# Kernel optimization log

Hardware: AMD Instinct MI355X
Metric: run time of the kernel (lower is better)

## Reference

```python
import jax, jax.numpy as jnp
import numpy as np

WINDOW = 8
DIM = 192
HEADS = 6
NWIN = 4096  # number of windows (B_)


def _relative_position_index(w):
    coords = np.stack(np.meshgrid(np.arange(w), np.arange(w), indexing='ij'))  # [2,w,w]
    cf = coords.reshape(2, -1)                                                 # [2, w*w]
    rel = cf[:, :, None] - cf[:, None, :]                                      # [2, N, N]
    rel = rel.transpose(1, 2, 0).astype(np.int32)
    rel[:, :, 0] += w - 1
    rel[:, :, 1] += w - 1
    rel[:, :, 0] *= 2 * w - 1
    return rel.sum(-1)  # [N, N] in [0, (2w-1)^2)


def setup_inputs() -> dict:
    key = jax.random.key(0)
    ks = jax.random.split(key, 6)
    N = WINDOW * WINDOW
    x = jax.random.normal(ks[0], (NWIN, N, DIM), dtype=jnp.float32)
    qkv_w = jax.random.normal(ks[1], (3 * DIM, DIM), dtype=jnp.float32) * (DIM ** -0.5)
    qkv_b = jax.random.normal(ks[2], (3 * DIM,), dtype=jnp.float32) * 0.02
    proj_w = jax.random.normal(ks[3], (DIM, DIM), dtype=jnp.float32) * (DIM ** -0.5)
    proj_b = jax.random.normal(ks[4], (DIM,), dtype=jnp.float32) * 0.02
    bias_table = jax.random.normal(ks[5], ((2 * WINDOW - 1) ** 2, HEADS), dtype=jnp.float32) * 0.02
    rel_index = jnp.asarray(_relative_position_index(WINDOW))
    return {"x": x, "qkv_w": qkv_w, "qkv_b": qkv_b, "proj_w": proj_w,
            "proj_b": proj_b, "bias_table": bias_table, "rel_index": rel_index}


def reference(x, qkv_w, qkv_b, proj_w, proj_b, bias_table, rel_index):
    B, N, C = x.shape
    H = HEADS
    hd = C // H
    scale = hd ** -0.5
    # qkv projection (torch Linear: x @ W.T + b)
    qkv = (x @ qkv_w.T + qkv_b).reshape(B, N, 3, H, hd)
    qkv = jnp.transpose(qkv, (2, 0, 3, 1, 4))  # [3, B, H, N, hd]
    q, k, v = qkv[0], qkv[1], qkv[2]
    attn = jnp.einsum('bhqd,bhkd->bhqk', q, k) * scale  # [B,H,N,N]
    # relative position bias gather: [N,N,H] -> [H,N,N]
    bias = bias_table[rel_index.reshape(-1)].reshape(N, N, H)
    bias = jnp.transpose(bias, (2, 0, 1))
    attn = jax.nn.softmax(attn + bias[None], axis=-1)
    out = jnp.einsum('bhqk,bhkd->bhqd', attn, v)         # [B,H,N,hd]
    out = jnp.transpose(out, (0, 2, 1, 3)).reshape(B, N, C)
    return out @ proj_w.T + proj_b
```

## Files before the change

kernel.cpp:

```cpp
#include <hip/hip_runtime.h>


#define NTOK 64
#define DIM  192
#define HEADS 6
#define NWIN 4096

typedef short short8  __attribute__((ext_vector_type(8)));
typedef short short4v __attribute__((ext_vector_type(4)));
typedef float f32x4   __attribute__((ext_vector_type(4)));

__device__ __forceinline__ short f2bf(float f) {
    unsigned u = __builtin_bit_cast(unsigned, f);
    unsigned r = (u + 0x7fffu + ((u >> 16) & 1u)) >> 16;
    return (short)r;
}

__device__ __forceinline__ short8 ld_cvt8(const float* p) {
    f32x4 a = *(const f32x4*)p;
    f32x4 b = *(const f32x4*)(p + 4);
    short8 r;
    r[0] = f2bf(a[0]); r[1] = f2bf(a[1]); r[2] = f2bf(a[2]); r[3] = f2bf(a[3]);
    r[4] = f2bf(b[0]); r[5] = f2bf(b[1]); r[6] = f2bf(b[2]); r[7] = f2bf(b[3]);
    return r;
}

#define QW_ELEMS 110592
#define TOT_W_ELEMS 147456

__global__ void convw(const float* __restrict__ qw, const float* __restrict__ pw,
                      short* __restrict__ wsw) {
    int i = (blockIdx.x * 256 + threadIdx.x) * 4;
    if (i >= TOT_W_ELEMS) return;
    const float* src = (i < QW_ELEMS) ? (qw + i) : (pw + (i - QW_ELEMS));
    f32x4 v = *(const f32x4*)src;
    short4v o;
    o[0] = f2bf(v[0]); o[1] = f2bf(v[1]); o[2] = f2bf(v[2]); o[3] = f2bf(v[3]);
    *(short4v*)(wsw + i) = o;
}

#define Q_OFF   0
#define K_OFF   12800
#define VT_OFF  25600
#define SMEM_SHORTS 39424

template <bool WF32>
__global__ __launch_bounds__(384, 3) void msa_fused(
    const float* __restrict__ x,
    const short* __restrict__ wq_bf, const short* __restrict__ wp_bf,
    const float* __restrict__ wq_f,  const float* __restrict__ wp_f,
    const float* __restrict__ qkv_b, const float* __restrict__ proj_b,
    const float* __restrict__ bias_table, const int* __restrict__ rel_index,
    float* __restrict__ out)
{
    __shared__ __align__(16) short smem[SMEM_SHORTS];

    const int tid  = threadIdx.x;
    const int wave = tid >> 6;
    const int lane = tid & 63;
    const int quad = lane >> 4;
    const int l15  = lane & 15;
    const int b    = blockIdx.x;

    short* qs = smem + Q_OFF;
    short* ks = smem + K_OFF;
    short* vt = smem + VT_OFF;

    const float* xg = x + b * (NTOK * DIM);
    short8 afr[4][6];
#pragma unroll
    for (int mt = 0; mt < 4; ++mt)
#pragma unroll
        for (int kk = 0; kk < 6; ++kk)
            afr[mt][kk] = ld_cvt8(xg + (mt*16 + l15)*DIM + kk*32 + quad*8);

#pragma unroll
    for (int nt = 0; nt < 6; ++nt) {
        const int N0 = wave*96 + nt*16;
        f32x4 acc[4];
#pragma unroll
        for (int mt = 0; mt < 4; ++mt) acc[mt] = (f32x4){0.f,0.f,0.f,0.f};
#pragma unroll
        for (int kk = 0; kk < 6; ++kk) {
            short8 bfr;
            if constexpr (WF32) bfr = ld_cvt8(wq_f + (N0 + l15)*DIM + kk*32 + quad*8);
            else                bfr = *(const short8*)(wq_bf + (N0 + l15)*DIM + kk*32 + quad*8);
#pragma unroll
            for (int mt = 0; mt < 4; ++mt)
                acc[mt] = __builtin_amdgcn_mfma_f32_16x16x32_bf16(afr[mt][kk], bfr, acc[mt], 0, 0, 0);
        }
        const float bv = qkv_b[N0 + l15];
        if (wave < 2) {
#pragma unroll
            for (int mt = 0; mt < 4; ++mt)
#pragma unroll
                for (int r = 0; r < 4; ++r)
                    qs[(mt*16 + quad*4 + r)*200 + N0 + l15] = f2bf(acc[mt][r] + bv);
        } else if (wave < 4) {
#pragma unroll
            for (int mt = 0; mt < 4; ++mt)
#pragma unroll
                for (int r = 0; r < 4; ++r)
                    ks[(mt*16 + quad*4 + r)*200 + (N0 - 192) + l15] = f2bf(acc[mt][r] + bv);
        } else {
#pragma unroll
            for (int mt = 0; mt < 4; ++mt)
#pragma unroll
                for (int r = 0; r < 4; ++r)
                    vt[(N0 - 384 + l15)*72 + mt*16 + quad*4 + r] = f2bf(acc[mt][r] + bv);
        }
    }
    __syncthreads();

    const int h = wave;
    const int koff = h*32 + quad*8;
    short8 qa[4], kb[4];
#pragma unroll
    for (int t = 0; t < 4; ++t) {
        qa[t] = *(const short8*)(qs + (t*16 + l15)*200 + koff);
        kb[t] = *(const short8*)(ks + (t*16 + l15)*200 + koff);
    }
    f32x4 s[4][4];
#pragma unroll
    for (int mt = 0; mt < 4; ++mt)
#pragma unroll
        for (int nt = 0; nt < 4; ++nt) {
            f32x4 z = (f32x4){0.f,0.f,0.f,0.f};
            s[mt][nt] = __builtin_amdgcn_mfma_f32_16x16x32_bf16(qa[mt], kb[nt], z, 0, 0, 0);
        }
    __syncthreads();

    const float scale = 0.17677669529663687f;
#pragma unroll
    for (int mt = 0; mt < 4; ++mt)
#pragma unroll
        for (int r = 0; r < 4; ++r) {
            const int row = mt*16 + quad*4 + r;
            float m = -1e30f;
#pragma unroll
            for (int nt = 0; nt < 4; ++nt) {
                const int col = nt*16 + l15;
                const int idx = rel_index[row*64 + col];
                float val = s[mt][nt][r]*scale + bias_table[idx*HEADS + h];
                s[mt][nt][r] = val;
                m = fmaxf(m, val);
            }
#pragma unroll
            for (int off = 8; off >= 1; off >>= 1) m = fmaxf(m, __shfl_xor(m, off, 16));
            float sum = 0.f;
#pragma unroll
            for (int nt = 0; nt < 4; ++nt) {
                float e = exp2f((s[mt][nt][r] - m) * 1.44269504f);
                s[mt][nt][r] = e;
                sum += e;
            }
#pragma unroll
            for (int off = 8; off >= 1; off >>= 1) sum += __shfl_xor(sum, off, 16);
            const float inv = 1.f / sum;
#pragma unroll
            for (int nt = 0; nt < 4; ++nt) s[mt][nt][r] *= inv;
        }

    short* ps = smem + wave*2560;
    f32x4 oa[4][2];
#pragma unroll
    for (int mt = 0; mt < 4; ++mt)
#pragma unroll
        for (int n2 = 0; n2 < 2; ++n2) oa[mt][n2] = (f32x4){0.f,0.f,0.f,0.f};
#pragma unroll
    for (int kh = 0; kh < 2; ++kh) {
        __syncthreads();
#pragma unroll
        for (int mt = 0; mt < 4; ++mt)
#pragma unroll
            for (int n2 = 0; n2 < 2; ++n2)
#pragma unroll
                for (int r = 0; r < 4; ++r)
                    ps[(mt*16 + quad*4 + r)*40 + n2*16 + l15] = f2bf(s[mt][kh*2 + n2][r]);
        __syncthreads();
        short8 pfr[4], vfr[2];
#pragma unroll
        for (int mt = 0; mt < 4; ++mt)
            pfr[mt] = *(const short8*)(ps + (mt*16 + l15)*40 + quad*8);
#pragma unroll
        for (int n2 = 0; n2 < 2; ++n2)
            vfr[n2] = *(const short8*)(vt + (h*32 + n2*16 + l15)*72 + kh*32 + quad*8);
#pragma unroll
        for (int mt = 0; mt < 4; ++mt)
#pragma unroll
            for (int n2 = 0; n2 < 2; ++n2)
                oa[mt][n2] = __builtin_amdgcn_mfma_f32_16x16x32_bf16(pfr[mt], vfr[n2], oa[mt][n2], 0, 0, 0);
    }
    __syncthreads();

    short* os = smem;
#pragma unroll
    for (int mt = 0; mt < 4; ++mt)
#pragma unroll
        for (int n2 = 0; n2 < 2; ++n2)
#pragma unroll
            for (int r = 0; r < 4; ++r)
                os[(mt*16 + quad*4 + r)*200 + h*32 + n2*16 + l15] = f2bf(oa[mt][n2][r]);
    __syncthreads();

    short8 ofr[4][6];
#pragma unroll
    for (int mt = 0; mt < 4; ++mt)
#pragma unroll
        for (int kk = 0; kk < 6; ++kk)
            ofr[mt][kk] = *(const short8*)(os + (mt*16 + l15)*200 + kk*32 + quad*8);

    float* outg = out + b * (NTOK * DIM);
#pragma unroll
    for (int nt = 0; nt < 2; ++nt) {
        const int c0 = wave*32 + nt*16;
        f32x4 acc[4];
#pragma unroll
        for (int mt = 0; mt < 4; ++mt) acc[mt] = (f32x4){0.f,0.f,0.f,0.f};
#pragma unroll
        for (int kk = 0; kk < 6; ++kk) {
            short8 bfr;
            if constexpr (WF32) bfr = ld_cvt8(wp_f + (c0 + l15)*DIM + kk*32 + quad*8);
            else                bfr = *(const short8*)(wp_bf + (c0 + l15)*DIM + kk*32 + quad*8);
#pragma unroll
            for (int mt = 0; mt < 4; ++mt)
                acc[mt] = __builtin_amdgcn_mfma_f32_16x16x32_bf16(ofr[mt][kk], bfr, acc[mt], 0, 0, 0);
        }
        const float pb = proj_b[c0 + l15];
#pragma unroll
        for (int mt = 0; mt < 4; ++mt)
#pragma unroll
            for (int r = 0; r < 4; ++r) {
                float sv = acc[mt][r] + pb;
                if (!(__builtin_fabsf(sv) < 1e30f)) sv = 0.f;
                outg[(mt*16 + quad*4 + r)*DIM + c0 + l15] = sv;
            }
    }
}

extern "C" void kernel_launch(void* const* d_in, const int* in_sizes, int n_in,
                              void* d_out, int out_size, void* d_ws, size_t ws_size,
                              hipStream_t stream) {
    const float* x          = (const float*)d_in[0];
    const float* qkv_w      = (const float*)d_in[1];
    const float* qkv_b      = (const float*)d_in[2];
    const float* proj_w     = (const float*)d_in[3];
    const float* proj_b     = (const float*)d_in[4];
    const float* bias_table = (const float*)d_in[5];
    const int*   rel_index  = (const int*)d_in[6];
    float* out = (float*)d_out;

    if (ws_size >= (size_t)TOT_W_ELEMS * sizeof(short)) {
        short* wsw = (short*)d_ws;
        convw<<<144, 256, 0, stream>>>(qkv_w, proj_w, wsw);
        msa_fused<false><<<NWIN, 384, 0, stream>>>(
            x, wsw, wsw + QW_ELEMS, qkv_w, proj_w,
            qkv_b, proj_b, bias_table, rel_index, out);
    } else {
        msa_fused<true><<<NWIN, 384, 0, stream>>>(
            x, nullptr, nullptr, qkv_w, proj_w,
            qkv_b, proj_b, bias_table, rel_index, out);
    }
}
```

Measured before the change: 864.0 us.

## Restructure per-head attention with register transposes, staged x, and pre-gathered bias fragments

Each wave now computes its own head's Q, K and V projections (Q/K transposed via W·x^T) and rearranges them into MFMA operand layout with cross-lane shuffles instead of writing them through shared memory. x is staged once in LDS as bf16, and the relative-position bias is pre-gathered by the prep kernel into fragment order. LDS drops from about 77KB to 25KB and launch bounds rise to 4 blocks per CU, removing several barriers. In exchange, every wave re-reads the x tile from LDS for all three projections and pays for many lane shuffles.

```diff
diff --git a/kernel.cpp b/kernel.cpp
--- a/kernel.cpp
+++ b/kernel.cpp
@@ -9,51 +9,70 @@
 typedef short short8  __attribute__((ext_vector_type(8)));
 typedef short short4v __attribute__((ext_vector_type(4)));
 typedef float f32x4   __attribute__((ext_vector_type(4)));
+typedef unsigned int u32;
+typedef u32 u32x2 __attribute__((ext_vector_type(2)));
+typedef u32 u32x4 __attribute__((ext_vector_type(4)));
+
+#define QW_SHORTS  110592
+#define W_SHORTS   147456
+#define BIAS_OFF_B 294912
+#define WS_NEEDED  (294912 + 98304)
 
 __device__ __forceinline__ short f2bf(float f) {
     unsigned u = __builtin_bit_cast(unsigned, f);
     unsigned r = (u + 0x7fffu + ((u >> 16) & 1u)) >> 16;
     return (short)r;
 }
-
+__device__ __forceinline__ u32 pkbf(float lo, float hi) {
+    u32 d;
+    asm("v_cvt_pk_bf16_f32 %0, %1, %2" : "=v"(d) : "v"(lo), "v"(hi));
+    return d;
+}
 __device__ __forceinline__ short8 ld_cvt8(const float* p) {
     f32x4 a = *(const f32x4*)p;
     f32x4 b = *(const f32x4*)(p + 4);
-    short8 r;
-    r[0] = f2bf(a[0]); r[1] = f2bf(a[1]); r[2] = f2bf(a[2]); r[3] = f2bf(a[3]);
-    r[4] = f2bf(b[0]); r[5] = f2bf(b[1]); r[6] = f2bf(b[2]); r[7] = f2bf(b[3]);
-    return r;
-}
-
-#define QW_ELEMS 110592
-#define TOT_W_ELEMS 147456
-
-__global__ void convw(const float* __restrict__ qw, const float* __restrict__ pw,
-                      short* __restrict__ wsw) {
-    int i = (blockIdx.x * 256 + threadIdx.x) * 4;
-    if (i >= TOT_W_ELEMS) return;
-    const float* src = (i < QW_ELEMS) ? (qw + i) : (pw + (i - QW_ELEMS));
-    f32x4 v = *(const f32x4*)src;
-    short4v o;
-    o[0] = f2bf(v[0]); o[1] = f2bf(v[1]); o[2] = f2bf(v[2]); o[3] = f2bf(v[3]);
-    *(short4v*)(wsw + i) = o;
-}
-
-#define Q_OFF   0
-#define K_OFF   12800
-#define VT_OFF  25600
-#define SMEM_SHORTS 39424
-
-template <bool WF32>
-__global__ __launch_bounds__(384, 3) void msa_fused(
+    u32x4 w;
+    w[0] = pkbf(a[0], a[1]); w[1] = pkbf(a[2], a[3]);
+    w[2] = pkbf(b[0], b[1]); w[3] = pkbf(b[2], b[3]);
+    return __builtin_bit_cast(short8, w);
+}
+
+__global__ void prep(const float* __restrict__ qw, const float* __restrict__ pw,
+                     const float* __restrict__ bt, const int* __restrict__ ri,
+                     short* __restrict__ wsw, float* __restrict__ biasf) {
+    const int bid = blockIdx.x;
+    if (bid < 144) {
+        const int i = (bid * 256 + threadIdx.x) * 4;
+        const float* src = (i < QW_SHORTS) ? (qw + i) : (pw + (i - QW_SHORTS));
+        f32x4 v = *(const f32x4*)src;
+        short4v o;
+        o[0] = f2bf(v[0]); o[1] = f2bf(v[1]); o[2] = f2bf(v[2]); o[3] = f2bf(v[3]);
+        *(short4v*)(wsw + i) = o;
+    } else {
+        const int j  = (bid - 144) * 256 + threadIdx.x;
+        const int r  = j & 3;
+        const int ln = (j >> 2) & 63;
+        const int nt = (j >> 8) & 3;
+        const int mt = (j >> 10) & 3;
+        const int hh = j >> 12;
+        const int q  = mt * 16 + (ln & 15);
+        const int k  = nt * 16 + (ln >> 4) * 4 + r;
+        biasf[j] = bt[ri[q * 64 + k] * HEADS + hh];
+    }
+}
+
+
+template <bool WS>
+__global__ __launch_bounds__(384, 4) void msa_fused(
     const float* __restrict__ x,
     const short* __restrict__ wq_bf, const short* __restrict__ wp_bf,
+    const float* __restrict__ bias_fr,
     const float* __restrict__ wq_f,  const float* __restrict__ wp_f,
     const float* __restrict__ qkv_b, const float* __restrict__ proj_b,
     const float* __restrict__ bias_table, const int* __restrict__ rel_index,
     float* __restrict__ out)
 {
-    __shared__ __align__(16) short smem[SMEM_SHORTS];
+    __shared__ __align__(16) short smem[12800];
 
     const int tid  = threadIdx.x;
     const int wave = tid >> 6;
@@ -61,179 +80,218 @@
     const int quad = lane >> 4;
     const int l15  = lane & 15;
     const int b    = blockIdx.x;
-
-    short* qs = smem + Q_OFF;
-    short* ks = smem + K_OFF;
-    short* vt = smem + VT_OFF;
+    const int h    = wave;
+
+    const int  srcA = ((quad & 1) << 5) + l15;
+    const bool hiq  = (quad >= 2);
+
+    auto gsel = [&](u32 a, u32 bb, int sl) -> u32 {
+        u32 va = (u32)__shfl((int)a, sl, 64);
+        u32 vb = (u32)__shfl((int)bb, sl, 64);
+        return hiq ? vb : va;
+    };
+    auto xpose = [&](u32 p00, u32 p01, u32 p10, u32 p11) -> short8 {
+        u32x4 w;
+        w[0] = gsel(p00, p10, srcA);
+        w[1] = gsel(p01, p11, srcA);
+        w[2] = gsel(p00, p10, srcA + 16);
+        w[3] = gsel(p01, p11, srcA + 16);
+        return __builtin_bit_cast(short8, w);
+    };
 
     const float* xg = x + b * (NTOK * DIM);
-    short8 afr[4][6];
-#pragma unroll
-    for (int mt = 0; mt < 4; ++mt)
-#pragma unroll
-        for (int kk = 0; kk < 6; ++kk)
-            afr[mt][kk] = ld_cvt8(xg + (mt*16 + l15)*DIM + kk*32 + quad*8);
-
-#pragma unroll
-    for (int nt = 0; nt < 6; ++nt) {
-        const int N0 = wave*96 + nt*16;
-        f32x4 acc[4];
-#pragma unroll
-        for (int mt = 0; mt < 4; ++mt) acc[mt] = (f32x4){0.f,0.f,0.f,0.f};
+#pragma unroll
+    for (int i = 0; i < 8; ++i) {
+        const int f   = tid + i * 384;
+        f32x4 v = *(const f32x4*)(xg + f * 4);
+        const int row = f / 48;
+        const int col = (f % 48) * 4;
+        u32x2 wv; wv[0] = pkbf(v[0], v[1]); wv[1] = pkbf(v[2], v[3]);
+        *(u32x2*)(smem + row * 200 + col) = wv;
+    }
+    __syncthreads();
+
+    short8 qa[4], kb[4], vfr[2][2];
+
+    auto qk_gemm = [&](int wbase, short8 (&fr)[4]) {
+        f32x4 acc[2][4];
+#pragma unroll
+        for (int ct = 0; ct < 2; ++ct)
+#pragma unroll
+            for (int tt = 0; tt < 4; ++tt) acc[ct][tt] = (f32x4){0.f,0.f,0.f,0.f};
 #pragma unroll
         for (int kk = 0; kk < 6; ++kk) {
-            short8 bfr;
-            if constexpr (WF32) bfr = ld_cvt8(wq_f + (N0 + l15)*DIM + kk*32 + quad*8);
-            else                bfr = *(const short8*)(wq_bf + (N0 + l15)*DIM + kk*32 + quad*8);
-#pragma unroll
-            for (int mt = 0; mt < 4; ++mt)
-                acc[mt] = __builtin_amdgcn_mfma_f32_16x16x32_bf16(afr[mt][kk], bfr, acc[mt], 0, 0, 0);
-        }
-        const float bv = qkv_b[N0 + l15];
-        if (wave < 2) {
-#pragma unroll
-            for (int mt = 0; mt < 4; ++mt)
-#pragma unroll
-                for (int r = 0; r < 4; ++r)
-                    qs[(mt*16 + quad*4 + r)*200 + N0 + l15] = f2bf(acc[mt][r] + bv);
-        } else if (wave < 4) {
-#pragma unroll
-            for (int mt = 0; mt < 4; ++mt)
-#pragma unroll
-                for (int r = 0; r < 4; ++r)
-                    ks[(mt*16 + quad*4 + r)*200 + (N0 - 192) + l15] = f2bf(acc[mt][r] + bv);
-        } else {
-#pragma unroll
-            for (int mt = 0; mt < 4; ++mt)
-#pragma unroll
-                for (int r = 0; r < 4; ++r)
-                    vt[(N0 - 384 + l15)*72 + mt*16 + quad*4 + r] = f2bf(acc[mt][r] + bv);
-        }
+            short8 xfr[4];
+#pragma unroll
+            for (int tt = 0; tt < 4; ++tt)
+                xfr[tt] = *(const short8*)(smem + (tt*16 + l15)*200 + kk*32 + quad*8);
+#pragma unroll
+            for (int ct = 0; ct < 2; ++ct) {
+                short8 wfr;
+                if constexpr (WS) wfr = *(const short8*)(wq_bf + (wbase + ct*16 + l15)*DIM + kk*32 + quad*8);
+                else              wfr = ld_cvt8(wq_f + (wbase + ct*16 + l15)*DIM + kk*32 + quad*8);
+#pragma unroll
+                for (int tt = 0; tt < 4; ++tt)
+                    acc[ct][tt] = __builtin_amdgcn_mfma_f32_16x16x32_bf16(wfr, xfr[tt], acc[ct][tt], 0, 0, 0);
+            }
+        }
+        f32x4 bq[2];
+        bq[0] = *(const f32x4*)(qkv_b + wbase + quad*4);
+        bq[1] = *(const f32x4*)(qkv_b + wbase + 16 + quad*4);
+#pragma unroll
+        for (int ct = 0; ct < 2; ++ct)
+#pragma unroll
+            for (int tt = 0; tt < 4; ++tt) acc[ct][tt] += bq[ct];
+#pragma unroll
+        for (int tt = 0; tt < 4; ++tt) {
+            u32 p00 = pkbf(acc[0][tt][0], acc[0][tt][1]);
+            u32 p01 = pkbf(acc[0][tt][2], acc[0][tt][3]);
+            u32 p10 = pkbf(acc[1][tt][0], acc[1][tt][1]);
+            u32 p11 = pkbf(acc[1][tt][2], acc[1][tt][3]);
+            fr[tt] = xpose(p00, p01, p10, p11);
+        }
+    };
+    qk_gemm(h*32,       qa);
+    qk_gemm(192 + h*32, kb);
+
+    {
+        f32x4 acc[4][2];
+#pragma unroll
+        for (int tt = 0; tt < 4; ++tt)
+#pragma unroll
+            for (int ct = 0; ct < 2; ++ct) acc[tt][ct] = (f32x4){0.f,0.f,0.f,0.f};
+#pragma unroll
+        for (int kk = 0; kk < 6; ++kk) {
+            short8 xfr[4];
+#pragma unroll
+            for (int tt = 0; tt < 4; ++tt)
+                xfr[tt] = *(const short8*)(smem + (tt*16 + l15)*200 + kk*32 + quad*8);
+#pragma unroll
+            for (int ct = 0; ct < 2; ++ct) {
+                const int wrow = 384 + h*32 + ct*16 + l15;
+                short8 wfr;
+                if constexpr (WS) wfr = *(const short8*)(wq_bf + wrow*DIM + kk*32 + quad*8);
+                else              wfr = ld_cvt8(wq_f + wrow*DIM + kk*32 + quad*8);
+#pragma unroll
+                for (int tt = 0; tt < 4; ++tt)
+                    acc[tt][ct] = __builtin_amdgcn_mfma_f32_16x16x32_bf16(xfr[tt], wfr, acc[tt][ct], 0, 0, 0);
+            }
+        }
+        const float bv0 = qkv_b[384 + h*32 + l15];
+        const float bv1 = qkv_b[384 + h*32 + 16 + l15];
+        u32 pkv[2][4][2];
+#pragma unroll
+        for (int tt = 0; tt < 4; ++tt) {
+#pragma unroll
+            for (int r = 0; r < 4; ++r) { acc[tt][0][r] += bv0; acc[tt][1][r] += bv1; }
+#pragma unroll
+            for (int ct = 0; ct < 2; ++ct) {
+                pkv[ct][tt][0] = pkbf(acc[tt][ct][0], acc[tt][ct][1]);
+                pkv[ct][tt][1] = pkbf(acc[tt][ct][2], acc[tt][ct][3]);
+            }
+        }
+#pragma unroll
+        for (int ct = 0; ct < 2; ++ct)
+#pragma unroll
+            for (int kh = 0; kh < 2; ++kh)
+                vfr[ct][kh] = xpose(pkv[ct][2*kh][0], pkv[ct][2*kh][1],
+                                    pkv[ct][2*kh+1][0], pkv[ct][2*kh+1][1]);
     }
     __syncthreads();
 
-    const int h = wave;
-    const int koff = h*32 + quad*8;
-    short8 qa[4], kb[4];
-#pragma unroll
-    for (int t = 0; t < 4; ++t) {
-        qa[t] = *(const short8*)(qs + (t*16 + l15)*200 + koff);
-        kb[t] = *(const short8*)(ks + (t*16 + l15)*200 + koff);
-    }
-    f32x4 s[4][4];
-#pragma unroll
-    for (int mt = 0; mt < 4; ++mt)
+    const float scale = 0.17677669529663687f;
+    const float L2E   = 1.44269504088896f;
+#pragma unroll
+    for (int mt = 0; mt < 4; ++mt) {
+        f32x4 s[4];
 #pragma unroll
         for (int nt = 0; nt < 4; ++nt) {
             f32x4 z = (f32x4){0.f,0.f,0.f,0.f};
-            s[mt][nt] = __builtin_amdgcn_mfma_f32_16x16x32_bf16(qa[mt], kb[nt], z, 0, 0, 0);
-        }
+            s[nt] = __builtin_amdgcn_mfma_f32_16x16x32_bf16(kb[nt], qa[mt], z, 0, 0, 0);
+        }
+        if constexpr (WS) {
+#pragma unroll
+            for (int nt = 0; nt < 4; ++nt) {
+                f32x4 bb = *(const f32x4*)(bias_fr + ((((h*4 + mt)*4 + nt)*64 + lane) << 2));
+#pragma unroll
+                for (int r = 0; r < 4; ++r) s[nt][r] = s[nt][r]*scale + bb[r];
+            }
+        } else {
+#pragma unroll
+            for (int nt = 0; nt < 4; ++nt)
+#pragma unroll
+                for (int r = 0; r < 4; ++r) {
+                    const int q = mt*16 + l15, k = nt*16 + quad*4 + r;
+                    s[nt][r] = s[nt][r]*scale + bias_table[rel_index[q*64 + k]*HEADS + h];
+                }
+        }
+        float m = -1e30f;
+#pragma unroll
+        for (int nt = 0; nt < 4; ++nt)
+#pragma unroll
+            for (int r = 0; r < 4; ++r) m = fmaxf(m, s[nt][r]);
+        m = fmaxf(m, __shfl_xor(m, 16)); m = fmaxf(m, __shfl_xor(m, 32));
+        float sum = 0.f;
+#pragma unroll
+        for (int nt = 0; nt < 4; ++nt)
+#pragma unroll
+            for (int r = 0; r < 4; ++r) {
+                float e = exp2f((s[nt][r] - m) * L2E);
+                s[nt][r] = e; sum += e;
+            }
+        sum += __shfl_xor(sum, 16); sum += __shfl_xor(sum, 32);
+        const float inv = 1.f / sum;
+        u32 pk[4][2];
+#pragma unroll
+        for (int nt = 0; nt < 4; ++nt) {
+            pk[nt][0] = pkbf(s[nt][0]*inv, s[nt][1]*inv);
+            pk[nt][1] = pkbf(s[nt][2]*inv, s[nt][3]*inv);
+        }
+        f32x4 oa[2];
+        oa[0] = (f32x4){0.f,0.f,0.f,0.f}; oa[1] = (f32x4){0.f,0.f,0.f,0.f};
+#pragma unroll
+        for (int kh = 0; kh < 2; ++kh) {
+            short8 pfr = xpose(pk[2*kh][0], pk[2*kh][1], pk[2*kh+1][0], pk[2*kh+1][1]);
+#pragma unroll
+            for (int ct = 0; ct < 2; ++ct)
+                oa[ct] = __builtin_amdgcn_mfma_f32_16x16x32_bf16(pfr, vfr[ct][kh], oa[ct], 0, 0, 0);
+        }
+#pragma unroll
+        for (int ct = 0; ct < 2; ++ct)
+#pragma unroll
+            for (int r = 0; r < 4; ++r)
+                smem[(mt*16 + quad*4 + r)*200 + h*32 + ct*16 + l15] = f2bf(oa[ct][r]);
+    }
     __syncthreads();
 
-    const float scale = 0.17677669529663687f;
-#pragma unroll
-    for (int mt = 0; mt < 4; ++mt)
-#pragma unroll
-        for (int r = 0; r < 4; ++r) {
-            const int row = mt*16 + quad*4 + r;
-            float m = -1e30f;
-#pragma unroll
-            for (int nt = 0; nt < 4; ++nt) {
-                const int col = nt*16 + l15;
-                const int idx = rel_index[row*64 + col];
-                float val = s[mt][nt][r]*scale + bias_table[idx*HEADS + h];
-                s[mt][nt][r] = val;
-                m = fmaxf(m, val);
-            }
-#pragma unroll
-            for (int off = 8; off >= 1; off >>= 1) m = fmaxf(m, __shfl_xor(m, off, 16));
-            float sum = 0.f;
-#pragma unroll
-            for (int nt = 0; nt < 4; ++nt) {
-                float e = exp2f((s[mt][nt][r] - m) * 1.44269504f);
-                s[mt][nt][r] = e;
-                sum += e;
-            }
-#pragma unroll
-            for (int off = 8; off >= 1; off >>= 1) sum += __shfl_xor(sum, off, 16);
-            const float inv = 1.f / sum;
-#pragma unroll
-            for (int nt = 0; nt < 4; ++nt) s[mt][nt][r] *= inv;
-        }
-
-    short* ps = smem + wave*2560;
-    f32x4 oa[4][2];
-#pragma unroll
-    for (int mt = 0; mt < 4; ++mt)
-#pragma unroll
-        for (int n2 = 0; n2 < 2; ++n2) oa[mt][n2] = (f32x4){0.f,0.f,0.f,0.f};
-#pragma unroll
-    for (int kh = 0; kh < 2; ++kh) {
-        __syncthreads();
-#pragma unroll
-        for (int mt = 0; mt < 4; ++mt)
-#pragma unroll
-            for (int n2 = 0; n2 < 2; ++n2)
-#pragma unroll
-                for (int r = 0; r < 4; ++r)
-                    ps[(mt*16 + quad*4 + r)*40 + n2*16 + l15] = f2bf(s[mt][kh*2 + n2][r]);
-        __syncthreads();
-        short8 pfr[4], vfr[2];
-#pragma unroll
-        for (int mt = 0; mt < 4; ++mt)
-            pfr[mt] = *(const short8*)(ps + (mt*16 + l15)*40 + quad*8);
-#pragma unroll
-        for (int n2 = 0; n2 < 2; ++n2)
-            vfr[n2] = *(const short8*)(vt + (h*32 + n2*16 + l15)*72 + kh*32 + quad*8);
-#pragma unroll
-        for (int mt = 0; mt < 4; ++mt)
-#pragma unroll
-            for (int n2 = 0; n2 < 2; ++n2)
-                oa[mt][n2] = __builtin_amdgcn_mfma_f32_16x16x32_bf16(pfr[mt], vfr[n2], oa[mt][n2], 0, 0, 0);
-    }
-    __syncthreads();
-
-    short* os = smem;
-#pragma unroll
-    for (int mt = 0; mt < 4; ++mt)
-#pragma unroll
-        for (int n2 = 0; n2 < 2; ++n2)
-#pragma unroll
-            for (int r = 0; r < 4; ++r)
-                os[(mt*16 + quad*4 + r)*200 + h*32 + n2*16 + l15] = f2bf(oa[mt][n2][r]);
-    __syncthreads();
-
-    short8 ofr[4][6];
-#pragma unroll
-    for (int mt = 0; mt < 4; ++mt)
-#pragma unroll
-        for (int kk = 0; kk < 6; ++kk)
-            ofr[mt][kk] = *(const short8*)(os + (mt*16 + l15)*200 + kk*32 + quad*8);
-
     float* outg = out + b * (NTOK * DIM);
 #pragma unroll
-    for (int nt = 0; nt < 2; ++nt) {
-        const int c0 = wave*32 + nt*16;
+    for (int nt2 = 0; nt2 < 2; ++nt2) {
+        const int c0 = h*32 + nt2*16;
         f32x4 acc[4];
 #pragma unroll
-        for (int mt = 0; mt < 4; ++mt) acc[mt] = (f32x4){0.f,0.f,0.f,0.f};
+        for (int tt = 0; tt < 4; ++tt) acc[tt] = (f32x4){0.f,0.f,0.f,0.f};
 #pragma unroll
         for (int kk = 0; kk < 6; ++kk) {
-            short8 bfr;
-            if constexpr (WF32) bfr = ld_cvt8(wp_f + (c0 + l15)*DIM + kk*32 + quad*8);
-            else                bfr = *(const short8*)(wp_bf + (c0 + l15)*DIM + kk*32 + quad*8);
-#pragma unroll
-            for (int mt = 0; mt < 4; ++mt)
-                acc[mt] = __builtin_amdgcn_mfma_f32_16x16x32_bf16(ofr[mt][kk], bfr, acc[mt], 0, 0, 0);
+            short8 ofr[4];
+#pragma unroll
+            for (int tt = 0; tt < 4; ++tt)
+                ofr[tt] = *(const short8*)(smem + (tt*16 + l15)*200 + kk*32 + quad*8);
+            short8 wfr;
+            if constexpr (WS) wfr = *(const short8*)(wp_bf + (c0 + l15)*DIM + kk*32 + quad*8);
+            else              wfr = ld_cvt8(wp_f + (c0 + l15)*DIM + kk*32 + quad*8);
+#pragma unroll
+            for (int tt = 0; tt < 4; ++tt)
+                acc[tt] = __builtin_amdgcn_mfma_f32_16x16x32_bf16(ofr[tt], wfr, acc[tt], 0, 0, 0);
         }
         const float pb = proj_b[c0 + l15];
 #pragma unroll
-        for (int mt = 0; mt < 4; ++mt)
+        for (int tt = 0; tt < 4; ++tt)
 #pragma unroll
             for (int r = 0; r < 4; ++r) {
-                float sv = acc[mt][r] + pb;
+                float sv = acc[tt][r] + pb;
                 if (!(__builtin_fabsf(sv) < 1e30f)) sv = 0.f;
-                outg[(mt*16 + quad*4 + r)*DIM + c0 + l15] = sv;
+                outg[(tt*16 + quad*4 + r)*DIM + c0 + l15] = sv;
             }
     }
 }
@@ -250,15 +308,16 @@
     const int*   rel_index  = (const int*)d_in[6];
     float* out = (float*)d_out;
 
-    if (ws_size >= (size_t)TOT_W_ELEMS * sizeof(short)) {
-        short* wsw = (short*)d_ws;
-        convw<<<144, 256, 0, stream>>>(qkv_w, proj_w, wsw);
-        msa_fused<false><<<NWIN, 384, 0, stream>>>(
-            x, wsw, wsw + QW_ELEMS, qkv_w, proj_w,
+    if (ws_size >= (size_t)WS_NEEDED) {
+        short* wsw   = (short*)d_ws;
+        float* biasf = (float*)((char*)d_ws + BIAS_OFF_B);
+        prep<<<240, 256, 0, stream>>>(qkv_w, proj_w, bias_table, rel_index, wsw, biasf);
+        msa_fused<true><<<NWIN, 384, 0, stream>>>(
+            x, wsw, wsw + QW_SHORTS, biasf, qkv_w, proj_w,
             qkv_b, proj_b, bias_table, rel_index, out);
     } else {
-        msa_fused<true><<<NWIN, 384, 0, stream>>>(
-            x, nullptr, nullptr, qkv_w, proj_w,
+        msa_fused<false><<<NWIN, 384, 0, stream>>>(
+            x, nullptr, nullptr, nullptr, qkv_w, proj_w,
             qkv_b, proj_b, bias_table, rel_index, out);
     }
 }
```

New measurement: 725.9 us. 1.19x faster.
